# Optimization experiments

Hardware: AMD Instinct MI355X
Metric: run time of the kernel (lower is better)

Reference implementation:

```python
import jax, jax.numpy as jnp
import numpy as np

D_MODEL = 1024
NUM_HEADS = 16
D_K = D_MODEL // NUM_HEADS


def setup_inputs() -> dict:
    key = jax.random.key(0)
    ks = jax.random.split(key, 6)
    B, S = 2, 2048
    scale = 1.0 / np.sqrt(D_MODEL)
    x = jax.random.normal(ks[0], (B, S, D_MODEL), dtype=jnp.float32)
    w_q = jax.random.normal(ks[1], (D_MODEL, D_MODEL), dtype=jnp.float32) * scale
    w_k = jax.random.normal(ks[2], (D_MODEL, D_MODEL), dtype=jnp.float32) * scale
    w_v = jax.random.normal(ks[3], (D_MODEL, D_MODEL), dtype=jnp.float32) * scale
    w_o = jax.random.normal(ks[4], (D_MODEL, D_MODEL), dtype=jnp.float32) * scale
    b_o = jax.random.normal(ks[5], (D_MODEL,), dtype=jnp.float32) * 0.01
    return {"x": x, "w_q": w_q, "w_k": w_k, "w_v": w_v, "w_o": w_o, "b_o": b_o}


def reference(x, w_q, w_k, w_v, w_o, b_o):
    B, S, _ = x.shape
    # Linear(d, d, bias=False): y = x @ W.T ; weights stored torch-style [out, in]
    def proj(w):
        y = jnp.einsum('bsd,ed->bse', x, w)
        return y.reshape(B, S, NUM_HEADS, D_K).transpose(0, 2, 1, 3)  # [B,H,S,Dk]
    Q, K, V = proj(w_q), proj(w_k), proj(w_v)
    scores = jnp.einsum('bhqd,bhkd->bhqk', Q, K) / np.sqrt(D_K)
    attn = jax.nn.softmax(scores, axis=-1)  # dropout p=0 (eval) -> identity
    out = jnp.einsum('bhqk,bhkd->bhqd', attn, V)
    out = out.transpose(0, 2, 1, 3).reshape(B, S, D_MODEL)
    return jnp.einsum('bsd,ed->bse', out, w_o) + b_o
```

## Files before the change

### kernel.cpp

```cpp
#include <hip/hip_runtime.h>
#include <hip/hip_bf16.h>


typedef __bf16 bf16x8 __attribute__((ext_vector_type(8)));
typedef float f32x4 __attribute__((ext_vector_type(4)));
typedef float f32x16 __attribute__((ext_vector_type(16)));

__device__ __forceinline__ unsigned short f2bf(float f) {
  union { float f; unsigned int u; } c; c.f = f;
  unsigned int u = c.u;
  return (unsigned short)((u + 0x7FFFu + ((u >> 16) & 1u)) >> 16);
}

__device__ __forceinline__ unsigned int cvtpk(float a, float b) {
  unsigned int r;
  asm("v_cvt_pk_bf16_f32 %0, %1, %2" : "=v"(r) : "v"(a), "v"(b));
  return r;
}

__device__ __forceinline__ bf16x8 ld_frag(const unsigned short* p) {
  union { uint4 u; bf16x8 b; } c;
  c.u = *(const uint4*)p;
  return c.b;
}

__device__ __forceinline__ uint4 cvt8(const float* __restrict__ p) {
  float4 a = *(const float4*)p;
  float4 b = *(const float4*)(p + 4);
  union { uint4 u; unsigned short s[8]; } r;
  r.s[0] = f2bf(a.x); r.s[1] = f2bf(a.y); r.s[2] = f2bf(a.z); r.s[3] = f2bf(a.w);
  r.s[4] = f2bf(b.x); r.s[5] = f2bf(b.y); r.s[6] = f2bf(b.z); r.s[7] = f2bf(b.w);
  return r.u;
}

typedef __attribute__((address_space(1))) const unsigned int as1_u32;
typedef __attribute__((address_space(3))) unsigned int as3_u32;
__device__ __forceinline__ void async16(const unsigned short* g,
                                        unsigned short* l) {
  __builtin_amdgcn_global_load_lds(
      (as1_u32*)(unsigned long long)g,
      (as3_u32*)(unsigned int)(unsigned long long)l, 16, 0, 0);
}

__global__ __launch_bounds__(256) void cvt_all(
    const float* __restrict__ s0, const float* __restrict__ s1,
    const float* __restrict__ s2, const float* __restrict__ s3,
    const float* __restrict__ s4,
    unsigned short* __restrict__ d0, unsigned short* __restrict__ d1,
    unsigned short* __restrict__ d2, unsigned short* __restrict__ d3,
    unsigned short* __restrict__ d4) {
  const float* srcs[5] = {s0, s1, s2, s3, s4};
  unsigned short* dsts[5] = {d0, d1, d2, d3, d4};
  const int ns[5] = {4194304, 1048576, 1048576, 1048576, 1048576};
  const int y = blockIdx.y;
  const int idx = (blockIdx.x * 256 + threadIdx.x) * 8;
  if (idx >= ns[y]) return;
  *(uint4*)(dsts[y] + idx) = cvt8(srcs[y] + idx);
}

template <bool OUT_F32>
__global__ __launch_bounds__(256, 4) void gemm_bt(
    const unsigned short* __restrict__ A,
    const unsigned short* __restrict__ w0,
    const unsigned short* __restrict__ w1,
    const unsigned short* __restrict__ w2,
    const float* __restrict__ bias,
    void* __restrict__ outraw, float z0scale) {
  const int z = blockIdx.z;
  const unsigned short* W = (z == 0) ? w0 : ((z == 1) ? w1 : w2);
  const float scl = (z == 0) ? z0scale : 1.0f;

  __shared__ unsigned short smem[(128 + 64) * 64];
  unsigned short* a_lds = smem;
  unsigned short* b_lds = smem + 128 * 64;

  const int tid = threadIdx.x;
  const int wave = tid >> 6, lane = tid & 63;
  const int quad = lane >> 4, l16 = lane & 15;
  const int wm = (wave >> 1) * 64, wn = (wave & 1) * 32;
  const int bm = blockIdx.x * 128, bn = blockIdx.y * 64;

  const int r8 = lane >> 3;
  const int sl = (lane & 7) ^ r8;
  const unsigned short* ga = A + (size_t)(bm + wave * 32 + r8) * 1024 + sl * 8;
  const unsigned short* gb = W + (size_t)(bn + wave * 16 + r8) * 1024 + sl * 8;
  unsigned short* la = &a_lds[wave * 32 * 64];
  unsigned short* lb = &b_lds[wave * 16 * 64];

  f32x4 acc[4][2] = {};

  for (int k0 = 0; k0 < 1024; k0 += 64) {
#pragma unroll
    for (int c = 0; c < 4; ++c)
      async16(ga + (size_t)c * 8 * 1024, la + c * 512);
#pragma unroll
    for (int c = 0; c < 2; ++c)
      async16(gb + (size_t)c * 8 * 1024, lb + c * 512);
    ga += 64; gb += 64;
    __syncthreads();

    bf16x8 af[2][4], bfr[2][2];
#pragma unroll
    for (int kk = 0; kk < 2; ++kk) {
#pragma unroll
      for (int t = 0; t < 4; ++t) {
        const int row = wm + t * 16 + l16;
        af[kk][t] =
            ld_frag(&a_lds[row * 64 + (((kk * 4 + quad) ^ (row & 7)) * 8)]);
      }
#pragma unroll
      for (int t = 0; t < 2; ++t) {
        const int row = wn + t * 16 + l16;
        bfr[kk][t] =
            ld_frag(&b_lds[row * 64 + (((kk * 4 + quad) ^ (row & 7)) * 8)]);
      }
    }
#pragma unroll
    for (int kk = 0; kk < 2; ++kk)
#pragma unroll
      for (int mt = 0; mt < 4; ++mt)
#pragma unroll
        for (int nt = 0; nt < 2; ++nt)
          acc[mt][nt] = __builtin_amdgcn_mfma_f32_16x16x32_bf16(
              af[kk][mt], bfr[kk][nt], acc[mt][nt], 0, 0, 0);
    __syncthreads();
  }

  if (!OUT_F32 && z == 2) {
    unsigned short* tt = smem;
#pragma unroll
    for (int nt = 0; nt < 2; ++nt) {
      const int d = wn + nt * 16 + l16;
#pragma unroll
      for (int mt = 0; mt < 4; ++mt) {
        const int ml = wm + mt * 16 + quad * 4;
        union { uint2 u; unsigned short s[4]; } pk;
#pragma unroll
        for (int r = 0; r < 4; ++r) pk.s[r] = f2bf(acc[mt][nt][r]);
        const int g = (ml >> 3) ^ (d & 7);
        *(uint2*)&tt[d * 128 + g * 8 + (ml & 7)] = pk.u;
      }
    }
    __syncthreads();
    const int d = tid >> 2, qtr = tid & 3;
    const int bb = bm >> 11, s0 = bm & 2047, hh = bn >> 6;
    unsigned short* vtp = (unsigned short*)outraw + (size_t)2 * 4096 * 1024 +
                          ((size_t)(bb * 16 + hh)) * 131072 +
                          (size_t)d * 2048 + s0 + qtr * 32;
#pragma unroll
    for (int k = 0; k < 4; ++k) {
      const int g = (qtr * 4 + k) ^ (d & 7);
      *(uint4*)&vtp[k * 8] = *(const uint4*)&tt[d * 128 + g * 8];
    }
    return;
  }

#pragma unroll
  for (int nt = 0; nt < 2; ++nt) {
    const int n = bn + wn + nt * 16 + l16;
    const float bv = bias ? bias[n] : 0.0f;
#pragma unroll
    for (int mt = 0; mt < 4; ++mt)
#pragma unroll
      for (int r = 0; r < 4; ++r) {
        const int m = bm + wm + mt * 16 + quad * 4 + r;
        const float v = acc[mt][nt][r] * scl + bv;
        if (OUT_F32)
          ((float*)outraw)[(size_t)z * 4096 * 1024 + (size_t)m * 1024 + n] = v;
        else
          ((unsigned short*)outraw)[(size_t)z * 4096 * 1024 +
                                    (size_t)m * 1024 + n] = f2bf(v);
      }
  }
}

__global__ __launch_bounds__(256, 4) void attn4(
    const unsigned short* __restrict__ qkv,
    const unsigned short* __restrict__ vt_g,
    unsigned short* __restrict__ ab) {
  constexpr size_t PL = (size_t)4096 * 1024;
  const int qt = blockIdx.x, bh = blockIdx.y;
  const int b = bh >> 4, h = bh & 15;

  __shared__ __align__(16) unsigned short kvs[2][2][64 * 64];
  __shared__ float sm_l[2][2][32];

  const int tid = threadIdx.x;
  const int wave = tid >> 6, lane = tid & 63;
  const int ws = wave >> 1, wq = wave & 1;
  const int hi = lane >> 5, l32 = lane & 31;
  const int row8 = lane >> 3;
  const int sl = (lane & 7) ^ (row8 & 7);
  const int swz = (l32 & 7) * 8;

  const unsigned short* qrow =
      qkv + (size_t)(b * 2048 + qt * 64 + wq * 32 + l32) * 1024 + h * 64 +
      hi * 8;
  bf16x8 qf[4];
#pragma unroll
  for (int kc = 0; kc < 4; ++kc) qf[kc] = ld_frag(qrow + kc * 16);

  const unsigned short* gK =
      qkv + PL + (size_t)(b * 2048 + ws * 1024 + wq * 32 + row8) * 1024 +
      h * 64 + sl * 8;
  const unsigned short* gV =
      vt_g + (size_t)bh * 64 * 2048 + (size_t)(wq * 32 + row8) * 2048 +
      ws * 1024 + sl * 8;
  unsigned short* lK = &kvs[ws][0][wq * 4 * 512];
  unsigned short* lV = &kvs[ws][1][wq * 4 * 512];

  f32x16 o_acc[2] = {};
  float l_part = 0.0f;

  for (int t = 0; t < 16; ++t) {
#pragma unroll
    for (int c = 0; c < 4; ++c) {
      async16(gK + (size_t)c * 8 * 1024, lK + c * 512);
      async16(gV + (size_t)c * 8 * 2048, lV + c * 512);
    }
    gK += 64 * 1024;
    gV += 64;
    __syncthreads();

    f32x16 st[2] = {};
#pragma unroll
    for (int mb = 0; mb < 2; ++mb)
#pragma unroll
      for (int kc = 0; kc < 4; ++kc) {
        bf16x8 ak = ld_frag(
            &kvs[ws][0][(mb * 32 + l32) * 64 + (((2 * kc + hi) * 8) ^ swz)]);
        st[mb] = __builtin_amdgcn_mfma_f32_32x32x16_bf16(ak, qf[kc], st[mb],
                                                         0, 0, 0);
      }

    unsigned int u[2][4][2];
#pragma unroll
    for (int mb = 0; mb < 2; ++mb) {
#pragma unroll
      for (int r = 0; r < 16; ++r) {
        const float p = __builtin_amdgcn_exp2f(st[mb][r]);
        st[mb][r] = p;
        l_part += p;
      }
#pragma unroll
      for (int g = 0; g < 4; ++g) {
        u[mb][g][0] = cvtpk(st[mb][g * 4 + 0], st[mb][g * 4 + 1]);
        u[mb][g][1] = cvtpk(st[mb][g * 4 + 2], st[mb][g * 4 + 3]);
      }
    }

#pragma unroll
    for (int ks = 0; ks < 4; ++ks) {
      const int m = ks >> 1, g = (ks & 1) * 2;
      unsigned int a0 = u[m][g][0], b0 = u[m][g + 1][0];
      unsigned int a1 = u[m][g][1], b1 = u[m][g + 1][1];
      asm("v_permlane32_swap_b32 %0, %1" : "+v"(a0), "+v"(b0));
      asm("v_permlane32_swap_b32 %0, %1" : "+v"(a1), "+v"(b1));
      union { unsigned int w[4]; bf16x8 f; } pa;
      pa.w[0] = a0; pa.w[1] = a1; pa.w[2] = b0; pa.w[3] = b1;
#pragma unroll
      for (int nb = 0; nb < 2; ++nb) {
        bf16x8 bv = ld_frag(
            &kvs[ws][1][(nb * 32 + l32) * 64 + (((2 * ks + hi) * 8) ^ swz)]);
        o_acc[nb] = __builtin_amdgcn_mfma_f32_32x32x16_bf16(pa.f, bv,
                                                            o_acc[nb], 0, 0, 0);
      }
    }
    __syncthreads();
  }

  float lsum = l_part + __shfl_xor(l_part, 32);

  float* sm_o = (float*)&kvs[0][0][0];
  if (ws == 1) {
#pragma unroll
    for (int nb = 0; nb < 2; ++nb)
#pragma unroll
      for (int r = 0; r < 16; ++r) {
        const int q = (r & 3) + 8 * (r >> 2) + 4 * hi;
        sm_o[wq * 2048 + q * 64 + nb * 32 + l32] = o_acc[nb][r];
      }
  }
  if (lane < 32) sm_l[ws][wq][l32] = lsum;
  __syncthreads();

  if (ws == 0) {
#pragma unroll
    for (int r = 0; r < 16; ++r) {
      const int q = (r & 3) + 8 * (r >> 2) + 4 * hi;
      const float inv = 1.0f / (sm_l[0][wq][q] + sm_l[1][wq][q]);
      const size_t row = (size_t)(b * 2048 + qt * 64 + wq * 32 + q);
#pragma unroll
      for (int nb = 0; nb < 2; ++nb) {
        const float v =
            (o_acc[nb][r] + sm_o[wq * 2048 + q * 64 + nb * 32 + l32]) * inv;
        ab[row * 1024 + h * 64 + nb * 32 + l32] = f2bf(v);
      }
    }
  }
}

extern "C" void kernel_launch(void* const* d_in, const int* in_sizes, int n_in,
                              void* d_out, int out_size, void* d_ws,
                              size_t ws_size, hipStream_t stream) {
  const float* x  = (const float*)d_in[0];
  const float* wq = (const float*)d_in[1];
  const float* wk = (const float*)d_in[2];
  const float* wv = (const float*)d_in[3];
  const float* wo = (const float*)d_in[4];
  const float* bo = (const float*)d_in[5];

  constexpr size_t PL = (size_t)4096 * 1024;
  unsigned short* qkv = (unsigned short*)d_ws;
  unsigned short* xb  = qkv + 3 * PL;
  unsigned short* ab  = xb;
  unsigned short* wqb = qkv + 4 * PL;
  unsigned short* wkb = wqb + 1024 * 1024;
  unsigned short* wvb = wkb + 1024 * 1024;
  unsigned short* wob = wvb + 1024 * 1024;

  const float QSCALE = 0.18033688011112042f;

  cvt_all<<<dim3(2048, 5), 256, 0, stream>>>(x, wq, wk, wv, wo,
                                             xb, wqb, wkb, wvb, wob);
  gemm_bt<false><<<dim3(32, 16, 3), 256, 0, stream>>>(
      xb, wqb, wkb, wvb, nullptr, qkv, QSCALE);
  attn4<<<dim3(32, 32), 256, 0, stream>>>(qkv, qkv + 2 * PL, ab);
  gemm_bt<true><<<dim3(32, 16, 1), 256, 0, stream>>>(
      ab, wob, wob, wob, bo, d_out, 1.0f);
}
```

Measured before the change: 185.6 us.

## Fuse QKV projections into one kernel sharing A tiles; widen output GEMM tile

The three Q/K/V projection GEMMs become one kernel in which each block loads its activation tile once and multiplies it against all three weight tiles, accumulating three sets of outputs. This cuts redundant global and LDS loads of the activation matrix. The output projection gets its own kernel with a 128x128 tile, raising per-block reuse. In exchange, register and LDS use per block grows and launch bounds drop occupancy to 2 and 3 blocks per CU, which can hurt latency hiding. The grid for the QKV GEMM also shrinks to 512 blocks.

```diff
diff --git a/kernel.cpp b/kernel.cpp
--- a/kernel.cpp
+++ b/kernel.cpp
@@ -58,19 +58,14 @@
   *(uint4*)(dsts[y] + idx) = cvt8(srcs[y] + idx);
 }
 
-template <bool OUT_F32>
-__global__ __launch_bounds__(256, 4) void gemm_bt(
+__global__ __launch_bounds__(256, 2) void gemm_qkv(
     const unsigned short* __restrict__ A,
     const unsigned short* __restrict__ w0,
     const unsigned short* __restrict__ w1,
     const unsigned short* __restrict__ w2,
-    const float* __restrict__ bias,
-    void* __restrict__ outraw, float z0scale) {
-  const int z = blockIdx.z;
-  const unsigned short* W = (z == 0) ? w0 : ((z == 1) ? w1 : w2);
-  const float scl = (z == 0) ? z0scale : 1.0f;
-
-  __shared__ unsigned short smem[(128 + 64) * 64];
+    unsigned short* __restrict__ out, float qscale) {
+  constexpr size_t PL = (size_t)4096 * 1024;
+  __shared__ unsigned short smem[(128 + 3 * 64) * 64];
   unsigned short* a_lds = smem;
   unsigned short* b_lds = smem + 128 * 64;
 
@@ -83,50 +78,76 @@
   const int r8 = lane >> 3;
   const int sl = (lane & 7) ^ r8;
   const unsigned short* ga = A + (size_t)(bm + wave * 32 + r8) * 1024 + sl * 8;
-  const unsigned short* gb = W + (size_t)(bn + wave * 16 + r8) * 1024 + sl * 8;
+  const unsigned short* gw0 = w0 + (size_t)(bn + wave * 16 + r8) * 1024 + sl * 8;
+  const unsigned short* gw1 = w1 + (size_t)(bn + wave * 16 + r8) * 1024 + sl * 8;
+  const unsigned short* gw2 = w2 + (size_t)(bn + wave * 16 + r8) * 1024 + sl * 8;
   unsigned short* la = &a_lds[wave * 32 * 64];
-  unsigned short* lb = &b_lds[wave * 16 * 64];
-
-  f32x4 acc[4][2] = {};
+  unsigned short* lb0 = &b_lds[0 * 4096 + wave * 16 * 64];
+  unsigned short* lb1 = &b_lds[1 * 4096 + wave * 16 * 64];
+  unsigned short* lb2 = &b_lds[2 * 4096 + wave * 16 * 64];
+
+  f32x4 acc[3][4][2] = {};
 
   for (int k0 = 0; k0 < 1024; k0 += 64) {
 #pragma unroll
     for (int c = 0; c < 4; ++c)
       async16(ga + (size_t)c * 8 * 1024, la + c * 512);
 #pragma unroll
-    for (int c = 0; c < 2; ++c)
-      async16(gb + (size_t)c * 8 * 1024, lb + c * 512);
-    ga += 64; gb += 64;
-    __syncthreads();
-
-    bf16x8 af[2][4], bfr[2][2];
+    for (int c = 0; c < 2; ++c) {
+      async16(gw0 + (size_t)c * 8 * 1024, lb0 + c * 512);
+      async16(gw1 + (size_t)c * 8 * 1024, lb1 + c * 512);
+      async16(gw2 + (size_t)c * 8 * 1024, lb2 + c * 512);
+    }
+    ga += 64; gw0 += 64; gw1 += 64; gw2 += 64;
+    __syncthreads();
+
 #pragma unroll
     for (int kk = 0; kk < 2; ++kk) {
+      bf16x8 af[4];
 #pragma unroll
       for (int t = 0; t < 4; ++t) {
         const int row = wm + t * 16 + l16;
-        af[kk][t] =
+        af[t] =
             ld_frag(&a_lds[row * 64 + (((kk * 4 + quad) ^ (row & 7)) * 8)]);
       }
 #pragma unroll
-      for (int t = 0; t < 2; ++t) {
-        const int row = wn + t * 16 + l16;
-        bfr[kk][t] =
-            ld_frag(&b_lds[row * 64 + (((kk * 4 + quad) ^ (row & 7)) * 8)]);
-      }
-    }
-#pragma unroll
-    for (int kk = 0; kk < 2; ++kk)
+      for (int z = 0; z < 3; ++z) {
+        bf16x8 bfr[2];
+#pragma unroll
+        for (int t = 0; t < 2; ++t) {
+          const int row = wn + t * 16 + l16;
+          bfr[t] = ld_frag(&b_lds[z * 4096 + row * 64 +
+                                  (((kk * 4 + quad) ^ (row & 7)) * 8)]);
+        }
+#pragma unroll
+        for (int mt = 0; mt < 4; ++mt)
+#pragma unroll
+          for (int nt = 0; nt < 2; ++nt)
+            acc[z][mt][nt] = __builtin_amdgcn_mfma_f32_16x16x32_bf16(
+                af[mt], bfr[nt], acc[z][mt][nt], 0, 0, 0);
+      }
+    }
+    __syncthreads();
+  }
+
+#pragma unroll
+  for (int z = 0; z < 2; ++z) {
+    const float scl = (z == 0) ? qscale : 1.0f;
+#pragma unroll
+    for (int nt = 0; nt < 2; ++nt) {
+      const int n = bn + wn + nt * 16 + l16;
 #pragma unroll
       for (int mt = 0; mt < 4; ++mt)
 #pragma unroll
-        for (int nt = 0; nt < 2; ++nt)
-          acc[mt][nt] = __builtin_amdgcn_mfma_f32_16x16x32_bf16(
-              af[kk][mt], bfr[kk][nt], acc[mt][nt], 0, 0, 0);
-    __syncthreads();
-  }
-
-  if (!OUT_F32 && z == 2) {
+        for (int r = 0; r < 4; ++r) {
+          const int m = bm + wm + mt * 16 + quad * 4 + r;
+          out[(size_t)z * PL + (size_t)m * 1024 + n] =
+              f2bf(acc[z][mt][nt][r] * scl);
+        }
+    }
+  }
+
+  {
     unsigned short* tt = smem;
 #pragma unroll
     for (int nt = 0; nt < 2; ++nt) {
@@ -136,7 +157,7 @@
         const int ml = wm + mt * 16 + quad * 4;
         union { uint2 u; unsigned short s[4]; } pk;
 #pragma unroll
-        for (int r = 0; r < 4; ++r) pk.s[r] = f2bf(acc[mt][nt][r]);
+        for (int r = 0; r < 4; ++r) pk.s[r] = f2bf(acc[2][mt][nt][r]);
         const int g = (ml >> 3) ^ (d & 7);
         *(uint2*)&tt[d * 128 + g * 8 + (ml & 7)] = pk.u;
       }
@@ -144,7 +165,7 @@
     __syncthreads();
     const int d = tid >> 2, qtr = tid & 3;
     const int bb = bm >> 11, s0 = bm & 2047, hh = bn >> 6;
-    unsigned short* vtp = (unsigned short*)outraw + (size_t)2 * 4096 * 1024 +
+    unsigned short* vtp = out + (size_t)2 * PL +
                           ((size_t)(bb * 16 + hh)) * 131072 +
                           (size_t)d * 2048 + s0 + qtr * 32;
 #pragma unroll
@@ -152,24 +173,75 @@
       const int g = (qtr * 4 + k) ^ (d & 7);
       *(uint4*)&vtp[k * 8] = *(const uint4*)&tt[d * 128 + g * 8];
     }
-    return;
-  }
-
-#pragma unroll
-  for (int nt = 0; nt < 2; ++nt) {
+  }
+}
+
+__global__ __launch_bounds__(256, 3) void gemm_out(
+    const unsigned short* __restrict__ A,
+    const unsigned short* __restrict__ W,
+    const float* __restrict__ bias, float* __restrict__ out) {
+  __shared__ unsigned short smem[256 * 64];
+  unsigned short* a_lds = smem;
+  unsigned short* b_lds = smem + 128 * 64;
+
+  const int tid = threadIdx.x;
+  const int wave = tid >> 6, lane = tid & 63;
+  const int quad = lane >> 4, l16 = lane & 15;
+  const int wm = (wave >> 1) * 64, wn = (wave & 1) * 64;
+  const int bm = blockIdx.x * 128, bn = blockIdx.y * 128;
+
+  const int r8 = lane >> 3;
+  const int sl = (lane & 7) ^ r8;
+  const unsigned short* ga = A + (size_t)(bm + wave * 32 + r8) * 1024 + sl * 8;
+  const unsigned short* gb = W + (size_t)(bn + wave * 32 + r8) * 1024 + sl * 8;
+  unsigned short* la = &a_lds[wave * 32 * 64];
+  unsigned short* lb = &b_lds[wave * 32 * 64];
+
+  f32x4 acc[4][4] = {};
+
+  for (int k0 = 0; k0 < 1024; k0 += 64) {
+#pragma unroll
+    for (int c = 0; c < 4; ++c) {
+      async16(ga + (size_t)c * 8 * 1024, la + c * 512);
+      async16(gb + (size_t)c * 8 * 1024, lb + c * 512);
+    }
+    ga += 64; gb += 64;
+    __syncthreads();
+
+    bf16x8 af[2][4], bfr[2][4];
+#pragma unroll
+    for (int kk = 0; kk < 2; ++kk) {
+#pragma unroll
+      for (int t = 0; t < 4; ++t) {
+        const int ra = wm + t * 16 + l16;
+        af[kk][t] =
+            ld_frag(&a_lds[ra * 64 + (((kk * 4 + quad) ^ (ra & 7)) * 8)]);
+        const int rb = wn + t * 16 + l16;
+        bfr[kk][t] =
+            ld_frag(&b_lds[rb * 64 + (((kk * 4 + quad) ^ (rb & 7)) * 8)]);
+      }
+    }
+#pragma unroll
+    for (int kk = 0; kk < 2; ++kk)
+#pragma unroll
+      for (int mt = 0; mt < 4; ++mt)
+#pragma unroll
+        for (int nt = 0; nt < 4; ++nt)
+          acc[mt][nt] = __builtin_amdgcn_mfma_f32_16x16x32_bf16(
+              af[kk][mt], bfr[kk][nt], acc[mt][nt], 0, 0, 0);
+    __syncthreads();
+  }
+
+#pragma unroll
+  for (int nt = 0; nt < 4; ++nt) {
     const int n = bn + wn + nt * 16 + l16;
-    const float bv = bias ? bias[n] : 0.0f;
+    const float bv = bias[n];
 #pragma unroll
     for (int mt = 0; mt < 4; ++mt)
 #pragma unroll
       for (int r = 0; r < 4; ++r) {
         const int m = bm + wm + mt * 16 + quad * 4 + r;
-        const float v = acc[mt][nt][r] * scl + bv;
-        if (OUT_F32)
-          ((float*)outraw)[(size_t)z * 4096 * 1024 + (size_t)m * 1024 + n] = v;
-        else
-          ((unsigned short*)outraw)[(size_t)z * 4096 * 1024 +
-                                    (size_t)m * 1024 + n] = f2bf(v);
+        out[(size_t)m * 1024 + n] = acc[mt][nt][r] + bv;
       }
   }
 }
@@ -323,9 +395,7 @@
 
   cvt_all<<<dim3(2048, 5), 256, 0, stream>>>(x, wq, wk, wv, wo,
                                              xb, wqb, wkb, wvb, wob);
-  gemm_bt<false><<<dim3(32, 16, 3), 256, 0, stream>>>(
-      xb, wqb, wkb, wvb, nullptr, qkv, QSCALE);
+  gemm_qkv<<<dim3(32, 16), 256, 0, stream>>>(xb, wqb, wkb, wvb, qkv, QSCALE);
   attn4<<<dim3(32, 32), 256, 0, stream>>>(qkv, qkv + 2 * PL, ab);
-  gemm_bt<true><<<dim3(32, 16, 1), 256, 0, stream>>>(
-      ab, wob, wob, wob, bo, d_out, 1.0f);
-}
+  gemm_out<<<dim3(32, 8), 256, 0, stream>>>(ab, wob, bo, (float*)d_out);
+}
```

Measured after the change: 185.8 us. Within noise of the previous version (+0.1%).
